# Kernel optimization log

Measured on AMD Instinct MI355X. Metric: run time of the kernel, lower is better.

The kernel has to match this reference:

```python
import jax, jax.numpy as jnp
import numpy as np


def _conv1x1(x, w, b):
    # x: (B,C,H,W), w: (O,C), b: (O,)
    return jnp.einsum('bchw,oc->bohw', x, w) + b[None, :, None, None]


def setup_inputs() -> dict:
    key = jax.random.key(0)
    ks = jax.random.split(key, 10)
    B, C, H, W = 8, 64, 64, 64
    x = jax.random.normal(ks[0], (B, C, H, W), dtype=jnp.float32)
    s = 0.05
    params = {}
    names = ['wq', 'wQ', 'wK', 'wV']
    for i, n in enumerate(names):
        params[n] = jax.random.normal(ks[1 + 2 * i], (C, C), dtype=jnp.float32) * s
        params['b' + n[1:]] = jax.random.normal(ks[2 + 2 * i], (C,), dtype=jnp.float32) * s
    return dict(x=x, wq=params['wq'], bq=params['bq'], wQ=params['wQ'], bQ=params['bQ'],
                wK=params['wK'], bK=params['bK'], wV=params['wV'], bV=params['bV'],
                gamma=jnp.ones((1,), dtype=jnp.float32))


def reference(x, wq, bq, wQ, bQ, wK, bK, wV, bV, gamma):
    B, C, H, W = x.shape
    # q = query_conv(x).view(B,-1,W,H)  (pure reshape, matches torch .view on contiguous tensor)
    q = _conv1x1(x, wq, bq).reshape(B, C, W, H)
    # 2x2 average pool, stride 2
    qp = q.reshape(B, C, W // 2, 2, H // 2, 2).mean(axis=(3, 5))
    q_ = qp.reshape(B, C, (W * H) // 4)          # (B, C, N/4)
    K = _conv1x1(x, wK, bK).reshape(B, C, H * W)  # (B, C, N)
    V = _conv1x1(x, wV, bV).reshape(B, C, H * W)  # (B, C, N)
    # stage 1: pooled queries attend over all keys
    attn1 = jax.nn.softmax(jnp.einsum('bcp,bcn->bpn', q_, K), axis=-1)  # (B, N/4, N)
    out = jnp.einsum('bcn,bpn->bcp', V, attn1)                           # (B, C, N/4)
    # stage 2: full queries attend over pooled anchors
    Q = _conv1x1(x, wQ, bQ).reshape(B, C, H * W)                         # (B, C, N)
    attn2 = jax.nn.softmax(jnp.einsum('bcn,bcp->bnp', Q, q_), axis=-1)   # (B, N, N/4)
    out = jnp.einsum('bcp,bnp->bcn', out, attn2)                         # (B, C, N)
    out = out.reshape(B, C, H, W)
    return gamma * out + x
```

## Files before the change

### kernel.cpp

```cpp
#include <hip/hip_runtime.h>
#include <hip/hip_bf16.h>


typedef float  f32x4  __attribute__((ext_vector_type(4)));
typedef float  f32x2  __attribute__((ext_vector_type(2)));
typedef __bf16 bf16x8 __attribute__((ext_vector_type(8)));
typedef __bf16 bf16x4 __attribute__((ext_vector_type(4)));

__device__ __forceinline__ int swz(int ch) { return ch ^ ((ch >> 3) & 7); }

__global__ __launch_bounds__(256) void conv4_kernel(
    const float* __restrict__ x,
    const float* __restrict__ wq, const float* __restrict__ bq,
    const float* __restrict__ wQ, const float* __restrict__ bQ,
    const float* __restrict__ wK, const float* __restrict__ bK,
    const float* __restrict__ wV, const float* __restrict__ bV,
    __bf16* __restrict__ Kt, __bf16* __restrict__ Vc,
    __bf16* __restrict__ Qt, __bf16* __restrict__ qt)
{
  __shared__ float xs[64 * 132];
  __shared__ float wsh[64 * 68];

  const int tid = threadIdx.x;
  const int m   = blockIdx.x >> 8;
  const int b   = (blockIdx.x >> 5) & 7;
  const int rp  = blockIdx.x & 31;
  const int n0  = rp << 7;

  const float* wg = (m == 0) ? wK : (m == 1) ? wV : (m == 2) ? wQ : wq;
  const float* bg = (m == 0) ? bK : (m == 1) ? bV : (m == 2) ? bQ : bq;

  for (int i = tid; i < 64 * 32; i += 256) {
    int c = i >> 5, j = i & 31;
    *(f32x4*)&xs[c * 132 + j * 4] =
        *(const f32x4*)&x[((size_t)(b * 64 + c)) * 4096 + n0 + j * 4];
  }
  for (int i = tid; i < 1024; i += 256) {
    int o = i >> 4, c0 = (i & 15) << 2;
    f32x4 v = *(const f32x4*)&wg[o * 64 + c0];
    wsh[(c0 + 0) * 68 + o] = v[0];
    wsh[(c0 + 1) * 68 + o] = v[1];
    wsh[(c0 + 2) * 68 + o] = v[2];
    wsh[(c0 + 3) * 68 + o] = v[3];
  }
  __syncthreads();

  const int ty = tid >> 4, tx = tid & 15;

  f32x2 acc2[4][4];
  {
    f32x4 bv = *(const f32x4*)&bg[ty * 4];
#pragma unroll
    for (int i = 0; i < 4; ++i)
#pragma unroll
      for (int j2 = 0; j2 < 4; ++j2) acc2[i][j2] = (f32x2){bv[i], bv[i]};
  }

#pragma unroll 4
  for (int c = 0; c < 64; ++c) {
    f32x4 wv = *(const f32x4*)&wsh[c * 68 + ty * 4];
    f32x4 xa = *(const f32x4*)&xs[c * 132 + tx * 8];
    f32x4 xb = *(const f32x4*)&xs[c * 132 + tx * 8 + 4];
    f32x2 xp[4] = {(f32x2){xa[0], xa[1]}, (f32x2){xa[2], xa[3]},
                   (f32x2){xb[0], xb[1]}, (f32x2){xb[2], xb[3]}};
#pragma unroll
    for (int i = 0; i < 4; ++i) {
      f32x2 wv2 = (f32x2){wv[i], wv[i]};
#pragma unroll
      for (int j2 = 0; j2 < 4; ++j2)
        acc2[i][j2] = __builtin_elementwise_fma(wv2, xp[j2], acc2[i][j2]);
    }
  }

  float acc[4][8];
#pragma unroll
  for (int i = 0; i < 4; ++i)
#pragma unroll
    for (int j = 0; j < 8; ++j) acc[i][j] = acc2[i][j >> 1][j & 1];

  if (m == 0 || m == 2) {
    __bf16* dst = (m == 0) ? Kt : Qt;
#pragma unroll
    for (int j = 0; j < 8; ++j) {
      int n = n0 + tx * 8 + j;
      bf16x4 pk;
#pragma unroll
      for (int i = 0; i < 4; ++i) pk[i] = (__bf16)acc[i][j];
      *(bf16x4*)&dst[((size_t)(b * 4096 + n)) * 64 + ty * 4] = pk;
    }
  } else if (m == 1) {
#pragma unroll
    for (int i = 0; i < 4; ++i) {
      int o = ty * 4 + i;
      bf16x8 pk;
#pragma unroll
      for (int j = 0; j < 8; ++j) pk[j] = (__bf16)acc[i][j];
      *(bf16x8*)&Vc[((size_t)(b * 64 + o)) * 4096 + n0 + tx * 8] = pk;
    }
  } else {
    float pl[4][4];
#pragma unroll
    for (int i = 0; i < 4; ++i)
#pragma unroll
      for (int jj = 0; jj < 4; ++jj)
        pl[i][jj] = acc[i][2 * jj] + acc[i][2 * jj + 1];
#pragma unroll
    for (int i = 0; i < 4; ++i)
#pragma unroll
      for (int jj = 0; jj < 4; ++jj)
        pl[i][jj] += __shfl_xor(pl[i][jj], 8);
    if (tx < 8) {
#pragma unroll
      for (int jj = 0; jj < 4; ++jj) {
        int p = rp * 32 + tx * 4 + jj;
        bf16x4 pk;
#pragma unroll
        for (int i = 0; i < 4; ++i) pk[i] = (__bf16)(0.25f * pl[i][jj]);
        *(bf16x4*)&qt[((size_t)(b * 1024 + p)) * 64 + ty * 4] = pk;
      }
    }
  }
}

__global__ __launch_bounds__(256, 2) void attn1_kernel(
    const __bf16* __restrict__ Qg,
    const __bf16* __restrict__ Kg,
    const __bf16* __restrict__ Vg,
    __bf16* __restrict__ partOb,
    float* __restrict__ partL)
{
  __shared__ __align__(16) char smem[40960];

  const int tid = threadIdx.x;
  const int w = tid >> 6, lane = tid & 63;
  const int lg = (lane >> 4) & 3, lp = lane & 15;
  const int b   = blockIdx.x >> 6;
  const int qb  = (blockIdx.x >> 4) & 3;
  const int ks  = blockIdx.x & 15;

  bf16x8 ones;
#pragma unroll
  for (int j = 0; j < 8; ++j) ones[j] = (__bf16)1.0f;

  bf16x8 qf[4][2];
#pragma unroll
  for (int qs = 0; qs < 4; ++qs) {
    const __bf16* qg =
        Qg + ((size_t)(b * 1024 + qb * 256 + w * 64 + qs * 16 + lp)) * 64;
    qf[qs][0] = *(const bf16x8*)(qg + lg * 8);
    qf[qs][1] = *(const bf16x8*)(qg + 32 + lg * 8);
  }

  f32x4 acc[4][4];
  f32x4 lacc[4];
#pragma unroll
  for (int qs = 0; qs < 4; ++qs) {
    lacc[qs] = (f32x4){0.f, 0.f, 0.f, 0.f};
#pragma unroll
    for (int ct = 0; ct < 4; ++ct) acc[qs][ct] = (f32x4){0.f, 0.f, 0.f, 0.f};
  }

  bf16x8 kreg[2], vreg[2];
  const int sw0 = swz(tid), sw1 = swz(tid + 256);
  auto load_tile = [&](int r) {
    const int kv0 = ks * 256 + r * 64;
#pragma unroll
    for (int j = 0; j < 2; ++j) {
      int s = tid + j * 256;
      kreg[j] = *(const bf16x8*)(Kg + ((size_t)(b * 4096 + kv0 + (s >> 3))) * 64 +
                                 (s & 7) * 8);
      vreg[j] = *(const bf16x8*)(Vg + ((size_t)(b * 64 + (s >> 3))) * 4096 + kv0 +
                                 (s & 7) * 8);
    }
  };
  auto write_tile = [&](int nb) {
    __bf16* kd = (__bf16*)(smem + nb * 8192);
    __bf16* vd = (__bf16*)(smem + 16384 + nb * 8192);
    *(bf16x8*)(kd + sw0 * 8) = kreg[0];
    *(bf16x8*)(kd + sw1 * 8) = kreg[1];
    *(bf16x8*)(vd + sw0 * 8) = vreg[0];
    *(bf16x8*)(vd + sw1 * 8) = vreg[1];
  };

  load_tile(0); write_tile(0); load_tile(1);
  __syncthreads();

  for (int r = 0; r < 4; ++r) {
    const int cur = r & 1;
    if (r + 1 < 4) write_tile(cur ^ 1);
    if (r + 2 < 4) load_tile(r + 2);

    const __bf16* lK = (const __bf16*)(smem + cur * 8192);
    const __bf16* lV = (const __bf16*)(smem + 16384 + cur * 8192);
    __bf16* lP = (__bf16*)(smem + 32768) + w * 1024;

    bf16x8 ka[4][2];
#pragma unroll
    for (int mt = 0; mt < 4; ++mt) {
      int ch0 = (mt * 16 + lp) * 8 + lg;
      ka[mt][0] = *(const bf16x8*)(lK + swz(ch0) * 8);
      ka[mt][1] = *(const bf16x8*)(lK + swz(ch0 + 4) * 8);
    }

    bf16x8 pf[4][2];
#pragma unroll
    for (int qs = 0; qs < 4; ++qs) {
      f32x4 S[4];
#pragma unroll
      for (int mt = 0; mt < 4; ++mt) {
        f32x4 z = (f32x4){0.f, 0.f, 0.f, 0.f};
        z = __builtin_amdgcn_mfma_f32_16x16x32_bf16(ka[mt][0], qf[qs][0], z, 0, 0, 0);
        z = __builtin_amdgcn_mfma_f32_16x16x32_bf16(ka[mt][1], qf[qs][1], z, 0, 0, 0);
        S[mt] = z;
      }

#pragma unroll
      for (int mt = 0; mt < 4; ++mt)
#pragma unroll
        for (int rr = 0; rr < 4; ++rr) S[mt][rr] = __expf(S[mt][rr]);

#pragma unroll
      for (int mt = 0; mt < 4; ++mt) {
        bf16x4 pk;
#pragma unroll
        for (int rr = 0; rr < 4; ++rr) pk[rr] = (__bf16)S[mt][rr];
        int boff = lp * 128 + mt * 32 + lg * 8;
        *(bf16x4*)((char*)lP + (boff ^ ((lp & 7) << 4))) = pk;
      }
      {
        int chp = lp * 8 + lg;
        pf[qs][0] = *(const bf16x8*)(lP + swz(chp) * 8);
        pf[qs][1] = *(const bf16x8*)(lP + swz(chp + 4) * 8);
        lacc[qs] = __builtin_amdgcn_mfma_f32_16x16x32_bf16(pf[qs][0], ones, lacc[qs], 0, 0, 0);
        lacc[qs] = __builtin_amdgcn_mfma_f32_16x16x32_bf16(pf[qs][1], ones, lacc[qs], 0, 0, 0);
      }
    }

#pragma unroll
    for (int ct = 0; ct < 4; ++ct) {
      int chv = (ct * 16 + lp) * 8 + lg;
      bf16x8 v0 = *(const bf16x8*)(lV + swz(chv) * 8);
      bf16x8 v1 = *(const bf16x8*)(lV + swz(chv + 4) * 8);
#pragma unroll
      for (int qs = 0; qs < 4; ++qs) {
        acc[qs][ct] = __builtin_amdgcn_mfma_f32_16x16x32_bf16(pf[qs][0], v0, acc[qs][ct], 0, 0, 0);
        acc[qs][ct] = __builtin_amdgcn_mfma_f32_16x16x32_bf16(pf[qs][1], v1, acc[qs][ct], 0, 0, 0);
      }
    }
    __syncthreads();
  }

  const int gq = w * 64;
  const size_t pbase = (size_t)((b * 4 + qb) * 16 + ks);
  if (lp == 0) {
#pragma unroll
    for (int qs = 0; qs < 4; ++qs)
      *(f32x4*)&partL[pbase * 256 + gq + qs * 16 + lg * 4] = lacc[qs];
  }
  __bf16* po = partOb + pbase * 16384;
#pragma unroll
  for (int qs = 0; qs < 4; ++qs)
#pragma unroll
    for (int ct = 0; ct < 4; ++ct) {
      bf16x4 pk;
#pragma unroll
      for (int rr = 0; rr < 4; ++rr) pk[rr] = (__bf16)acc[qs][ct][rr];
      *(bf16x4*)&po[(ct * 16 + lp) * 256 + gq + qs * 16 + lg * 4] = pk;
    }
}

__global__ __launch_bounds__(256) void combine1_kernel(
    const __bf16* __restrict__ partOb, const float* __restrict__ partL,
    __bf16* __restrict__ O1)
{
  __shared__ float linv[256];

  const int tid = threadIdx.x;
  const int b   = blockIdx.x >> 5;
  const int qb  = (blockIdx.x >> 3) & 3;
  const int cs  = blockIdx.x & 7;
  const size_t rbase = (size_t)((b * 4 + qb) * 16);

  {
    float l = 0.f;
#pragma unroll
    for (int s = 0; s < 16; ++s) l += partL[(rbase + s) * 256 + tid];
    linv[tid] = 1.0f / l;
  }
  __syncthreads();

  const int c = cs * 8 + (tid >> 5), q8 = (tid & 31) * 8;
  float o[8] = {0.f, 0.f, 0.f, 0.f, 0.f, 0.f, 0.f, 0.f};
#pragma unroll
  for (int s = 0; s < 16; ++s) {
    bf16x8 v = *(const bf16x8*)(partOb + (rbase + s) * 16384 + c * 256 + q8);
#pragma unroll
    for (int j = 0; j < 8; ++j) o[j] += (float)v[j];
  }
  bf16x8 pk;
#pragma unroll
  for (int j = 0; j < 8; ++j) pk[j] = (__bf16)(o[j] * linv[q8 + j]);
  *(bf16x8*)(O1 + ((size_t)(b * 64 + c)) * 1024 + qb * 256 + q8) = pk;
}

__global__ __launch_bounds__(512, 2) void attn2_kernel(
    const __bf16* __restrict__ Qg,
    const __bf16* __restrict__ Kg,
    const __bf16* __restrict__ Vg,
    float* __restrict__ outp,
    const float* __restrict__ xres,
    const float* __restrict__ gammap)
{
  __shared__ __align__(16) char smem[81920];

  const int tid = threadIdx.x;
  const int w = tid >> 6, lane = tid & 63;
  const int lg = (lane >> 4) & 3, lp = lane & 15;
  const int qg4 = w & 3, ks = w >> 2;
  const int b  = blockIdx.x >> 5;
  const int q0 = (blockIdx.x & 31) * 128;

  bf16x8 ones;
#pragma unroll
  for (int j = 0; j < 8; ++j) ones[j] = (__bf16)1.0f;

  bf16x8 qf[2][2];
#pragma unroll
  for (int qs = 0; qs < 2; ++qs) {
    const __bf16* qg =
        Qg + ((size_t)(b * 4096 + q0 + qg4 * 32 + qs * 16 + lp)) * 64;
    qf[qs][0] = *(const bf16x8*)(qg + lg * 8);
    qf[qs][1] = *(const bf16x8*)(qg + 32 + lg * 8);
  }

  f32x4 acc[2][4];
  f32x4 lacc[2];
#pragma unroll
  for (int qs = 0; qs < 2; ++qs) {
    lacc[qs] = (f32x4){0.f, 0.f, 0.f, 0.f};
#pragma unroll
    for (int ct = 0; ct < 4; ++ct) acc[qs][ct] = (f32x4){0.f, 0.f, 0.f, 0.f};
  }

  bf16x8 kreg[2], vreg[2];
  const int csi = tid & 255, sp = tid >> 8;
  const int sw0 = swz(csi), sw1 = swz(csi + 256);
  auto load_tile = [&](int r) {
    const int a0 = sp * 512 + r * 64;
#pragma unroll
    for (int j = 0; j < 2; ++j) {
      int s = csi + j * 256;
      int row = s >> 3, col = (s & 7) * 8;
      kreg[j] = *(const bf16x8*)(Kg + ((size_t)(b * 1024 + a0 + row)) * 64 + col);
      vreg[j] = *(const bf16x8*)(Vg + ((size_t)(b * 64 + row)) * 1024 + a0 + col);
    }
  };
  auto write_tile = [&](int nb) {
    __bf16* kd = (__bf16*)(smem + (sp * 2 + nb) * 8192);
    __bf16* vd = (__bf16*)(smem + 32768 + (sp * 2 + nb) * 8192);
    *(bf16x8*)(kd + sw0 * 8) = kreg[0];
    *(bf16x8*)(kd + sw1 * 8) = kreg[1];
    *(bf16x8*)(vd + sw0 * 8) = vreg[0];
    *(bf16x8*)(vd + sw1 * 8) = vreg[1];
  };

  load_tile(0); write_tile(0); load_tile(1);
  __syncthreads();

  for (int r = 0; r < 8; ++r) {
    const int cur = r & 1;
    if (r + 1 < 8) write_tile(cur ^ 1);
    if (r + 2 < 8) load_tile(r + 2);

    const __bf16* lK = (const __bf16*)(smem + (ks * 2 + cur) * 8192);
    const __bf16* lV = (const __bf16*)(smem + 32768 + (ks * 2 + cur) * 8192);
    __bf16* lP = (__bf16*)(smem + 65536) + w * 1024;

    bf16x8 ka[4][2];
#pragma unroll
    for (int mt = 0; mt < 4; ++mt) {
      int ch0 = (mt * 16 + lp) * 8 + lg;
      ka[mt][0] = *(const bf16x8*)(lK + swz(ch0) * 8);
      ka[mt][1] = *(const bf16x8*)(lK + swz(ch0 + 4) * 8);
    }

    bf16x8 pf[2][2];
#pragma unroll
    for (int qs = 0; qs < 2; ++qs) {
      f32x4 S[4];
#pragma unroll
      for (int mt = 0; mt < 4; ++mt) {
        f32x4 z = (f32x4){0.f, 0.f, 0.f, 0.f};
        z = __builtin_amdgcn_mfma_f32_16x16x32_bf16(ka[mt][0], qf[qs][0], z, 0, 0, 0);
        z = __builtin_amdgcn_mfma_f32_16x16x32_bf16(ka[mt][1], qf[qs][1], z, 0, 0, 0);
        S[mt] = z;
      }

#pragma unroll
      for (int mt = 0; mt < 4; ++mt)
#pragma unroll
        for (int rr = 0; rr < 4; ++rr) S[mt][rr] = __expf(S[mt][rr]);

#pragma unroll
      for (int mt = 0; mt < 4; ++mt) {
        bf16x4 pk;
#pragma unroll
        for (int rr = 0; rr < 4; ++rr) pk[rr] = (__bf16)S[mt][rr];
        int boff = lp * 128 + mt * 32 + lg * 8;
        *(bf16x4*)((char*)lP + (boff ^ ((lp & 7) << 4))) = pk;
      }
      {
        int chp = lp * 8 + lg;
        pf[qs][0] = *(const bf16x8*)(lP + swz(chp) * 8);
        pf[qs][1] = *(const bf16x8*)(lP + swz(chp + 4) * 8);
        lacc[qs] = __builtin_amdgcn_mfma_f32_16x16x32_bf16(pf[qs][0], ones, lacc[qs], 0, 0, 0);
        lacc[qs] = __builtin_amdgcn_mfma_f32_16x16x32_bf16(pf[qs][1], ones, lacc[qs], 0, 0, 0);
      }
    }

#pragma unroll
    for (int ct = 0; ct < 4; ++ct) {
      int chv = (ct * 16 + lp) * 8 + lg;
      bf16x8 v0 = *(const bf16x8*)(lV + swz(chv) * 8);
      bf16x8 v1 = *(const bf16x8*)(lV + swz(chv + 4) * 8);
#pragma unroll
      for (int qs = 0; qs < 2; ++qs) {
        acc[qs][ct] = __builtin_amdgcn_mfma_f32_16x16x32_bf16(pf[qs][0], v0, acc[qs][ct], 0, 0, 0);
        acc[qs][ct] = __builtin_amdgcn_mfma_f32_16x16x32_bf16(pf[qs][1], v1, acc[qs][ct], 0, 0, 0);
      }
    }
    __syncthreads();
  }

  float* cb = (float*)smem;
  float* lb = (float*)(smem + 73728);
  if (lp == 0) {
#pragma unroll
    for (int qs = 0; qs < 2; ++qs)
      *(f32x4*)(lb + w * 32 + qs * 16 + lg * 4) = lacc[qs];
  }
  {
    float* myc = cb + w * 2304;
#pragma unroll
    for (int qs = 0; qs < 2; ++qs)
#pragma unroll
      for (int ct = 0; ct < 4; ++ct)
        *(f32x4*)(myc + (ct * 16 + lp) * 36 + qs * 16 + lg * 4) = acc[qs][ct];
  }
  __syncthreads();

  if (w < 4) {
    const int g = w;
    const float g0 = gammap[0];
#pragma unroll
    for (int qs = 0; qs < 2; ++qs) {
      f32x4 lv0 = *(const f32x4*)(lb + g * 32 + qs * 16 + lg * 4);
      f32x4 lv1 = *(const f32x4*)(lb + (g + 4) * 32 + qs * 16 + lg * 4);
      f32x4 inv4;
#pragma unroll
      for (int j = 0; j < 4; ++j) inv4[j] = 1.0f / (lv0[j] + lv1[j]);
#pragma unroll
      for (int ct = 0; ct < 4; ++ct) {
        int coff = (ct * 16 + lp) * 36 + qs * 16 + lg * 4;
        f32x4 t0 = *(const f32x4*)(cb + g * 2304 + coff);
        f32x4 t1 = *(const f32x4*)(cb + (g + 4) * 2304 + coff);
        size_t oi = ((size_t)(b * 64 + ct * 16 + lp)) * 4096 + q0 + g * 32 +
                    qs * 16 + lg * 4;
        f32x4 xr = *(const f32x4*)(xres + oi);
        f32x4 res;
#pragma unroll
        for (int j = 0; j < 4; ++j)
          res[j] = g0 * ((t0[j] + t1[j]) * inv4[j]) + xr[j];
        *(f32x4*)(outp + oi) = res;
      }
    }
  }
}

extern "C" void kernel_launch(void* const* d_in, const int* in_sizes, int n_in,
                              void* d_out, int out_size, void* d_ws, size_t ws_size,
                              hipStream_t stream) {
  const float* x     = (const float*)d_in[0];
  const float* wq    = (const float*)d_in[1];
  const float* bq    = (const float*)d_in[2];
  const float* wQ    = (const float*)d_in[3];
  const float* bQ    = (const float*)d_in[4];
  const float* wK    = (const float*)d_in[5];
  const float* bK    = (const float*)d_in[6];
  const float* wV    = (const float*)d_in[7];
  const float* bV    = (const float*)d_in[8];
  const float* gamma = (const float*)d_in[9];

  __bf16* ws = (__bf16*)d_ws;
  __bf16* Kt = ws;
  __bf16* Vc = ws + 2097152;
  __bf16* Qt = ws + 4194304;
  __bf16* qt = ws + 6291456;
  __bf16* O1 = ws + 6815744;
  __bf16* partOb1 = (__bf16*)((char*)d_ws + (16ull << 20));
  float*  partL1  = (float*)((char*)d_ws + (33ull << 20));

  hipLaunchKernelGGL(conv4_kernel, dim3(1024), dim3(256), 0, stream,
                     x, wq, bq, wQ, bQ, wK, bK, wV, bV, Kt, Vc, Qt, qt);
  hipLaunchKernelGGL(attn1_kernel, dim3(512), dim3(256), 0, stream,
                     qt, Kt, Vc, partOb1, partL1);
  hipLaunchKernelGGL(combine1_kernel, dim3(256), dim3(256), 0, stream,
                     partOb1, partL1, O1);
  hipLaunchKernelGGL(attn2_kernel, dim3(256), dim3(512), 0, stream,
                     Qt, qt, O1, (float*)d_out, x, gamma);
}
```

Baseline: 65.66 us.

## Repartition attn2 warps into 2 query groups by 4 key splits

```diff
diff --git a/kernel.cpp b/kernel.cpp
--- a/kernel.cpp
+++ b/kernel.cpp
@@ -311,12 +311,12 @@
     const float* __restrict__ xres,
     const float* __restrict__ gammap)
 {
-  __shared__ __align__(16) char smem[81920];
+  __shared__ __align__(16) char smem[147456];
 
   const int tid = threadIdx.x;
   const int w = tid >> 6, lane = tid & 63;
   const int lg = (lane >> 4) & 3, lp = lane & 15;
-  const int qg4 = w & 3, ks = w >> 2;
+  const int qg4 = w & 1, ks = w >> 1;
   const int b  = blockIdx.x >> 5;
   const int q0 = (blockIdx.x & 31) * 128;
 
@@ -324,57 +324,57 @@
 #pragma unroll
   for (int j = 0; j < 8; ++j) ones[j] = (__bf16)1.0f;
 
-  bf16x8 qf[2][2];
-#pragma unroll
-  for (int qs = 0; qs < 2; ++qs) {
+  bf16x8 qf[4][2];
+#pragma unroll
+  for (int qs = 0; qs < 4; ++qs) {
     const __bf16* qg =
-        Qg + ((size_t)(b * 4096 + q0 + qg4 * 32 + qs * 16 + lp)) * 64;
+        Qg + ((size_t)(b * 4096 + q0 + qg4 * 64 + qs * 16 + lp)) * 64;
     qf[qs][0] = *(const bf16x8*)(qg + lg * 8);
     qf[qs][1] = *(const bf16x8*)(qg + 32 + lg * 8);
   }
 
-  f32x4 acc[2][4];
-  f32x4 lacc[2];
-#pragma unroll
-  for (int qs = 0; qs < 2; ++qs) {
+  f32x4 acc[4][4];
+  f32x4 lacc[4];
+#pragma unroll
+  for (int qs = 0; qs < 4; ++qs) {
     lacc[qs] = (f32x4){0.f, 0.f, 0.f, 0.f};
 #pragma unroll
     for (int ct = 0; ct < 4; ++ct) acc[qs][ct] = (f32x4){0.f, 0.f, 0.f, 0.f};
   }
 
-  bf16x8 kreg[2], vreg[2];
-  const int csi = tid & 255, sp = tid >> 8;
-  const int sw0 = swz(csi), sw1 = swz(csi + 256);
+  bf16x8 kreg[4], vreg[4];
+  const int swt = swz(tid);
   auto load_tile = [&](int r) {
-    const int a0 = sp * 512 + r * 64;
-#pragma unroll
-    for (int j = 0; j < 2; ++j) {
-      int s = csi + j * 256;
-      int row = s >> 3, col = (s & 7) * 8;
-      kreg[j] = *(const bf16x8*)(Kg + ((size_t)(b * 1024 + a0 + row)) * 64 + col);
-      vreg[j] = *(const bf16x8*)(Vg + ((size_t)(b * 64 + row)) * 1024 + a0 + col);
+#pragma unroll
+    for (int j = 0; j < 4; ++j) {
+      const int a0 = j * 256 + r * 64;
+      kreg[j] = *(const bf16x8*)(Kg + ((size_t)(b * 1024 + a0 + (tid >> 3))) * 64 +
+                                 (tid & 7) * 8);
+      vreg[j] = *(const bf16x8*)(Vg + ((size_t)(b * 64 + (tid >> 3))) * 1024 + a0 +
+                                 (tid & 7) * 8);
     }
   };
   auto write_tile = [&](int nb) {
-    __bf16* kd = (__bf16*)(smem + (sp * 2 + nb) * 8192);
-    __bf16* vd = (__bf16*)(smem + 32768 + (sp * 2 + nb) * 8192);
-    *(bf16x8*)(kd + sw0 * 8) = kreg[0];
-    *(bf16x8*)(kd + sw1 * 8) = kreg[1];
-    *(bf16x8*)(vd + sw0 * 8) = vreg[0];
-    *(bf16x8*)(vd + sw1 * 8) = vreg[1];
+#pragma unroll
+    for (int j = 0; j < 4; ++j) {
+      __bf16* kd = (__bf16*)(smem + (j * 2 + nb) * 8192);
+      __bf16* vd = (__bf16*)(smem + 65536 + (j * 2 + nb) * 8192);
+      *(bf16x8*)(kd + swt * 8) = kreg[j];
+      *(bf16x8*)(vd + swt * 8) = vreg[j];
+    }
   };
 
   load_tile(0); write_tile(0); load_tile(1);
   __syncthreads();
 
-  for (int r = 0; r < 8; ++r) {
+  for (int r = 0; r < 4; ++r) {
     const int cur = r & 1;
-    if (r + 1 < 8) write_tile(cur ^ 1);
-    if (r + 2 < 8) load_tile(r + 2);
+    if (r + 1 < 4) write_tile(cur ^ 1);
+    if (r + 2 < 4) load_tile(r + 2);
 
     const __bf16* lK = (const __bf16*)(smem + (ks * 2 + cur) * 8192);
-    const __bf16* lV = (const __bf16*)(smem + 32768 + (ks * 2 + cur) * 8192);
-    __bf16* lP = (__bf16*)(smem + 65536) + w * 1024;
+    const __bf16* lV = (const __bf16*)(smem + 65536 + (ks * 2 + cur) * 8192);
+    __bf16* lP = (__bf16*)(smem + 131072) + w * 1024;
 
     bf16x8 ka[4][2];
 #pragma unroll
@@ -384,9 +384,9 @@
       ka[mt][1] = *(const bf16x8*)(lK + swz(ch0 + 4) * 8);
     }
 
-    bf16x8 pf[2][2];
-#pragma unroll
-    for (int qs = 0; qs < 2; ++qs) {
+    bf16x8 pf[4][2];
+#pragma unroll
+    for (int qs = 0; qs < 4; ++qs) {
       f32x4 S[4];
 #pragma unroll
       for (int mt = 0; mt < 4; ++mt) {
@@ -424,7 +424,7 @@
       bf16x8 v0 = *(const bf16x8*)(lV + swz(chv) * 8);
       bf16x8 v1 = *(const bf16x8*)(lV + swz(chv + 4) * 8);
 #pragma unroll
-      for (int qs = 0; qs < 2; ++qs) {
+      for (int qs = 0; qs < 4; ++qs) {
         acc[qs][ct] = __builtin_amdgcn_mfma_f32_16x16x32_bf16(pf[qs][0], v0, acc[qs][ct], 0, 0, 0);
         acc[qs][ct] = __builtin_amdgcn_mfma_f32_16x16x32_bf16(pf[qs][1], v1, acc[qs][ct], 0, 0, 0);
       }
@@ -433,44 +433,50 @@
   }
 
   float* cb = (float*)smem;
-  float* lb = (float*)(smem + 73728);
+  float* lb = (float*)(smem + 139264);
   if (lp == 0) {
 #pragma unroll
-    for (int qs = 0; qs < 2; ++qs)
-      *(f32x4*)(lb + w * 32 + qs * 16 + lg * 4) = lacc[qs];
+    for (int qs = 0; qs < 4; ++qs)
+      *(f32x4*)(lb + (qg4 * 4 + ks) * 64 + qs * 16 + lg * 4) = lacc[qs];
   }
   {
-    float* myc = cb + w * 2304;
-#pragma unroll
-    for (int qs = 0; qs < 2; ++qs)
+    float* myc = cb + (size_t)(qg4 * 4 + ks) * 64 * 68;
+#pragma unroll
+    for (int qs = 0; qs < 4; ++qs)
 #pragma unroll
       for (int ct = 0; ct < 4; ++ct)
-        *(f32x4*)(myc + (ct * 16 + lp) * 36 + qs * 16 + lg * 4) = acc[qs][ct];
+        *(f32x4*)(myc + (ct * 16 + lp) * 68 + qs * 16 + lg * 4) = acc[qs][ct];
   }
   __syncthreads();
 
   if (w < 4) {
-    const int g = w;
+    const int g  = w & 1;
+    const int qh = w >> 1;
     const float g0 = gammap[0];
 #pragma unroll
-    for (int qs = 0; qs < 2; ++qs) {
-      f32x4 lv0 = *(const f32x4*)(lb + g * 32 + qs * 16 + lg * 4);
-      f32x4 lv1 = *(const f32x4*)(lb + (g + 4) * 32 + qs * 16 + lg * 4);
+    for (int qq = 0; qq < 2; ++qq) {
+      const int qs = qh * 2 + qq;
+      f32x4 lsum = (f32x4){0.f, 0.f, 0.f, 0.f};
+#pragma unroll
+      for (int s = 0; s < 4; ++s)
+        lsum += *(const f32x4*)(lb + (g * 4 + s) * 64 + qs * 16 + lg * 4);
       f32x4 inv4;
 #pragma unroll
-      for (int j = 0; j < 4; ++j) inv4[j] = 1.0f / (lv0[j] + lv1[j]);
+      for (int j = 0; j < 4; ++j) inv4[j] = 1.0f / lsum[j];
 #pragma unroll
       for (int ct = 0; ct < 4; ++ct) {
-        int coff = (ct * 16 + lp) * 36 + qs * 16 + lg * 4;
-        f32x4 t0 = *(const f32x4*)(cb + g * 2304 + coff);
-        f32x4 t1 = *(const f32x4*)(cb + (g + 4) * 2304 + coff);
-        size_t oi = ((size_t)(b * 64 + ct * 16 + lp)) * 4096 + q0 + g * 32 +
+        f32x4 t = (f32x4){0.f, 0.f, 0.f, 0.f};
+#pragma unroll
+        for (int s = 0; s < 4; ++s)
+          t += *(const f32x4*)(cb + ((size_t)(g * 4 + s) * 64 + ct * 16 + lp) * 68 +
+                               qs * 16 + lg * 4);
+        size_t oi = ((size_t)(b * 64 + ct * 16 + lp)) * 4096 + q0 + g * 64 +
                     qs * 16 + lg * 4;
         f32x4 xr = *(const f32x4*)(xres + oi);
         f32x4 res;
 #pragma unroll
         for (int j = 0; j < 4; ++j)
-          res[j] = g0 * ((t0[j] + t1[j]) * inv4[j]) + xr[j];
+          res[j] = g0 * (t[j] * inv4[j]) + xr[j];
         *(f32x4*)(outp + oi) = res;
       }
     }
```

Measured after the change: 65.61 us (median of 2 runs). Within noise of the previous version (-0.1%).
